# Optimization experiments

Measured on AMD Instinct MI355X. Metric: run time of the kernel, lower is better.

Reference implementation:

```python
import jax, jax.numpy as jnp
import numpy as np
from jax import lax

UP, DOWN, PAD, GAIN = 2, 1, 2, 4  # init_kwargs: up=2, down=1, padding=2 (symmetric), gain=4

def _make_filter():
    # filter = outer(f1d, f1d) / sum, matching torch ger + normalize
    f1 = jnp.asarray([1.0, 3.0, 3.0, 1.0], dtype=jnp.float32)
    f2 = jnp.outer(f1, f1)
    return f2 / jnp.sum(f2)

def setup_inputs() -> dict:
    key = jax.random.key(0)
    x = jax.random.normal(key, (8, 256, 128, 128), dtype=jnp.float32)
    return {"x": x, "f": _make_filter()}

def reference(x, f):
    # Faithful upfirdn2d: zero-insert upsample by UP, pad, depthwise FIR conv, stride-DOWN downsample.
    # Torch path: insert (UP-1) zeros AFTER each sample (length H*UP incl. trailing zeros), then pad
    # [PAD, PAD] per side. Equivalent fused form: lhs_dilation=UP (length (H-1)*UP+1, no trailing
    # zeros) with right pad = PAD + (UP-1). Strided-slice [::DOWN] after valid conv starting at 0
    # equals window_strides=DOWN. torch conv2d is cross-correlation, same as lax conv (no flip).
    C = x.shape[1]
    # gain scaling: f * gain ** (ndim/2) with ndim==2 -> f * gain
    w = jnp.tile((f * GAIN).astype(x.dtype)[None, None], (C, 1, 1, 1))  # (C,1,4,4) depthwise
    pad = ((PAD, PAD + UP - 1), (PAD, PAD + UP - 1))
    out = lax.conv_general_dilated(
        x, w,
        window_strides=(DOWN, DOWN),
        padding=pad,
        lhs_dilation=(UP, UP),
        dimension_numbers=("NCHW", "OIHW", "NCHW"),
        feature_group_count=C,
    )
    return out  # (8, 256, 257, 257)
```

## Files before the change

kernel.cpp:

```cpp
#include <hip/hip_runtime.h>


#define H_IN   128
#define W_IN   128
#define H_OUT  257
#define W_OUT  257
#define TOY    64
#define NROWS  (TOY/2 + 2)
#define LDW    136

__global__ __launch_bounds__(256) void upfirdn_kernel(const float* __restrict__ x,
                                                      float* __restrict__ out) {
    __shared__ alignas(16) float lds[NROWS * LDW];

    const int tid = threadIdx.x;
    const int nc  = blockIdx.y;
    const int oy0 = blockIdx.x * TOY;
    const int toy = min(TOY, H_OUT - oy0);
    const int nrows = ((toy - 1) >> 1) + ((toy - 1) & 1) + 2;

    const float* __restrict__ xin = x + (size_t)nc * (H_IN * W_IN);
    float* __restrict__ orow = out + (size_t)nc * (H_OUT * W_OUT) + (size_t)oy0 * W_OUT;

    const int iy_lo = (oy0 >> 1) - 1;

    for (int i = tid; i < nrows * (W_IN / 4); i += 256) {
        const int r  = i >> 5;
        const int c4 = (i & 31) << 2;
        const int iy = iy_lo + r;
        float4 v = make_float4(0.f, 0.f, 0.f, 0.f);
        if (iy >= 0 && iy < H_IN) {
            v = *reinterpret_cast<const float4*>(xin + iy * W_IN + c4);
        }
        *reinterpret_cast<float4*>(&lds[r * LDW + 4 + c4]) = v;
    }
    if (tid < nrows * 2) {
        const int r = tid >> 1;
        lds[r * LDW + ((tid & 1) ? 132 : 3)] = 0.f;
    }
    __syncthreads();

    {
        const int   ox  = tid;
        const float wx0 = (ox & 1) ? 0.75f : 0.25f;
        const float wx1 = (ox & 1) ? 0.25f : 0.75f;
        const float* bp = &lds[(ox >> 1) + (ox & 1) + 3];
        float h0 = bp[0]   * wx0 + bp[1]       * wx1;
        float h1 = bp[LDW] * wx0 + bp[LDW + 1] * wx1;
        float* o0 = orow + ox;
        const int npairs = toy >> 1;
        for (int k = 0; k < npairs; ++k) {
            const float* rp = bp + (k + 2) * LDW;
            const float h2 = rp[0] * wx0 + rp[1] * wx1;
            o0[(2 * k    ) * W_OUT] = h0 * 0.25f + h1 * 0.75f;
            o0[(2 * k + 1) * W_OUT] = h1 * 0.75f + h2 * 0.25f;
            h0 = h1; h1 = h2;
        }
        if (toy & 1) {
            o0[(toy - 1) * W_OUT] = h0 * 0.25f + h1 * 0.75f;
        }
    }

    for (int oyl = tid; oyl < toy; oyl += 256) {
        const int   ry0 = (oyl >> 1) + (oyl & 1);
        const float wy0 = (oyl & 1) ? 0.75f : 0.25f;
        const float wy1 = (oyl & 1) ? 0.25f : 0.75f;
        const float a = lds[ ry0      * LDW + 131];
        const float b = lds[(ry0 + 1) * LDW + 131];
        orow[oyl * W_OUT + 256] = (a * wy0 + b * wy1) * 0.25f;
    }
}

extern "C" void kernel_launch(void* const* d_in, const int* in_sizes, int n_in,
                              void* d_out, int out_size, void* d_ws, size_t ws_size,
                              hipStream_t stream) {
    const float* x = (const float*)d_in[0];
    float* out = (float*)d_out;

    const int n_tiles = (H_OUT + TOY - 1) / TOY;
    dim3 grid(n_tiles, 8 * 256, 1);
    dim3 block(256, 1, 1);
    upfirdn_kernel<<<grid, block, 0, stream>>>(x, out);
}
```

Measured before the change: 640.3 us.

## Precompute horizontal pass into LDS and write aligned float4 output rows

The horizontal 2x interpolation now runs during the global load, using wavefront shuffles for neighbour samples, and fills an LDS buffer of horizontally upsampled rows with a padded pitch and a bank-skew index. The vertical pass then writes output with 16-byte-aligned float4 stores, working out a per-row lead offset because the 257-wide rows are misaligned, plus scalar head and tail fixups. The aim is to replace scalar 4-byte strided stores with wide coalesced stores on this store-bound kernel. In exchange there are more LDS reads, serial fixup loops run by single lanes, and more complex indexing.

```diff
diff --git a/kernel.cpp b/kernel.cpp
--- a/kernel.cpp
+++ b/kernel.cpp
@@ -7,67 +7,81 @@
 #define W_OUT  257
 #define TOY    64
 #define NROWS  (TOY/2 + 2)
-#define LDW    136
+#define PITCH  265
+
+__device__ __forceinline__ int hidx(int ox) { return ox + (ox >> 5); }
 
 __global__ __launch_bounds__(256) void upfirdn_kernel(const float* __restrict__ x,
                                                       float* __restrict__ out) {
-    __shared__ alignas(16) float lds[NROWS * LDW];
+    __shared__ float H[NROWS * PITCH];
 
     const int tid = threadIdx.x;
     const int nc  = blockIdx.y;
     const int oy0 = blockIdx.x * TOY;
     const int toy = min(TOY, H_OUT - oy0);
     const int nrows = ((toy - 1) >> 1) + ((toy - 1) & 1) + 2;
+    const int iy_lo = (oy0 >> 1) - 1;
 
     const float* __restrict__ xin = x + (size_t)nc * (H_IN * W_IN);
     float* __restrict__ orow = out + (size_t)nc * (H_OUT * W_OUT) + (size_t)oy0 * W_OUT;
 
-    const int iy_lo = (oy0 >> 1) - 1;
-
-    for (int i = tid; i < nrows * (W_IN / 4); i += 256) {
-        const int r  = i >> 5;
-        const int c4 = (i & 31) << 2;
-        const int iy = iy_lo + r;
-        float4 v = make_float4(0.f, 0.f, 0.f, 0.f);
-        if (iy >= 0 && iy < H_IN) {
-            v = *reinterpret_cast<const float4*>(xin + iy * W_IN + c4);
+    {
+        const int g = tid & 31;
+        for (int i = tid; i < nrows * 32; i += 256) {
+            const int r  = i >> 5;
+            const int iy = iy_lo + r;
+            float4 v = make_float4(0.f, 0.f, 0.f, 0.f);
+            if (iy >= 0 && iy < H_IN)
+                v = *reinterpret_cast<const float4*>(xin + iy * W_IN + (g << 2));
+            float xm1 = __shfl_up(v.w, 1, 32);   if (g == 0)  xm1 = 0.f;
+            float xp4 = __shfl_down(v.x, 1, 32); if (g == 31) xp4 = 0.f;
+            float* hr = &H[r * PITCH + (g << 3) + (g >> 2)];
+            hr[0] = 0.25f * xm1 + 0.75f * v.x;
+            hr[1] = 0.75f * v.x + 0.25f * v.y;
+            hr[2] = 0.25f * v.x + 0.75f * v.y;
+            hr[3] = 0.75f * v.y + 0.25f * v.z;
+            hr[4] = 0.25f * v.y + 0.75f * v.z;
+            hr[5] = 0.75f * v.z + 0.25f * v.w;
+            hr[6] = 0.25f * v.z + 0.75f * v.w;
+            hr[7] = 0.75f * v.w + 0.25f * xp4;
+            if (g == 31) H[r * PITCH + hidx(256)] = 0.25f * v.w;
         }
-        *reinterpret_cast<float4*>(&lds[r * LDW + 4 + c4]) = v;
-    }
-    if (tid < nrows * 2) {
-        const int r = tid >> 1;
-        lds[r * LDW + ((tid & 1) ? 132 : 3)] = 0.f;
     }
     __syncthreads();
 
     {
-        const int   ox  = tid;
-        const float wx0 = (ox & 1) ? 0.75f : 0.25f;
-        const float wx1 = (ox & 1) ? 0.25f : 0.75f;
-        const float* bp = &lds[(ox >> 1) + (ox & 1) + 3];
-        float h0 = bp[0]   * wx0 + bp[1]       * wx1;
-        float h1 = bp[LDW] * wx0 + bp[LDW + 1] * wx1;
-        float* o0 = orow + ox;
-        const int npairs = toy >> 1;
-        for (int k = 0; k < npairs; ++k) {
-            const float* rp = bp + (k + 2) * LDW;
-            const float h2 = rp[0] * wx0 + rp[1] * wx1;
-            o0[(2 * k    ) * W_OUT] = h0 * 0.25f + h1 * 0.75f;
-            o0[(2 * k + 1) * W_OUT] = h1 * 0.75f + h2 * 0.25f;
-            h0 = h1; h1 = h2;
+        const int qg = tid & 63;
+        const int r4 = tid >> 6;
+        for (int j = 0; j < TOY / 4; ++j) {
+            const int row = (j << 2) + r4;
+            if (row >= toy) break;
+            const int   ry0 = (row >> 1) + (row & 1);
+            const float wy0 = (row & 1) ? 0.75f : 0.25f;
+            const float wy1 = 1.0f - wy0;
+            const float* h0 = &H[ry0 * PITCH];
+            const float* h1 = h0 + PITCH;
+            float* ro = orow + row * W_OUT;
+            const int lead = (-(nc + oy0 + row)) & 3;
+            const int gmax = (253 - lead) >> 2;
+            if (qg <= gmax) {
+                const int ox = lead + (qg << 2);
+                float4 o;
+                o.x = wy0 * h0[hidx(ox    )] + wy1 * h1[hidx(ox    )];
+                o.y = wy0 * h0[hidx(ox + 1)] + wy1 * h1[hidx(ox + 1)];
+                o.z = wy0 * h0[hidx(ox + 2)] + wy1 * h1[hidx(ox + 2)];
+                o.w = wy0 * h0[hidx(ox + 3)] + wy1 * h1[hidx(ox + 3)];
+                *reinterpret_cast<float4*>(ro + ox) = o;
+            }
+            if (qg == 0) {
+                for (int c = 0; c < lead; ++c)
+                    ro[c] = wy0 * h0[hidx(c)] + wy1 * h1[hidx(c)];
+            }
+            if (qg == 1) {
+                const int tstart = lead + ((gmax + 1) << 2);
+                for (int c = tstart; c <= 256; ++c)
+                    ro[c] = wy0 * h0[hidx(c)] + wy1 * h1[hidx(c)];
+            }
         }
-        if (toy & 1) {
-            o0[(toy - 1) * W_OUT] = h0 * 0.25f + h1 * 0.75f;
-        }
-    }
-
-    for (int oyl = tid; oyl < toy; oyl += 256) {
-        const int   ry0 = (oyl >> 1) + (oyl & 1);
-        const float wy0 = (oyl & 1) ? 0.75f : 0.25f;
-        const float wy1 = (oyl & 1) ? 0.25f : 0.75f;
-        const float a = lds[ ry0      * LDW + 131];
-        const float b = lds[(ry0 + 1) * LDW + 131];
-        orow[oyl * W_OUT + 256] = (a * wy0 + b * wy1) * 0.25f;
     }
 }
 
```

Measured after the change: 636.4 us. No clear change (-0.6%).
